# Kernel tuning notes

Hardware: AMD Instinct MI355X
Metric: run time of the kernel (lower is better)

The kernel has to match this reference:

```python
import jax, jax.numpy as jnp
import numpy as np

B, S, D, NH = 2, 1024, 2048, 8
QK, V, I = 1024, 2048, 8192  # qk_dim = D/2, v_dim = D, intermediate = 4D
CAP = 15.0
EPS = 1e-6


def setup_inputs() -> dict:
    key = jax.random.key(0)
    ks = jax.random.split(key, 12)
    sc = D ** -0.5
    return {
        "x": jax.random.normal(ks[0], (B, S, D), jnp.float32),
        "Wq": jax.random.normal(ks[1], (D, QK), jnp.float32) * sc,
        "Wk": jax.random.normal(ks[2], (D, QK), jnp.float32) * sc,
        "Wv": jax.random.normal(ks[3], (D, V), jnp.float32) * sc,
        "Wo": jax.random.normal(ks[4], (D, V), jnp.float32) * sc,
        "Wi": jax.random.normal(ks[5], (D, NH), jnp.float32) * sc,
        "bi": -10.0 * jnp.ones((NH,), jnp.float32),   # xLSTM input-gate bias init
        "Wf": jax.random.normal(ks[6], (D, NH), jnp.float32) * sc,
        "bf": jnp.linspace(3.0, 6.0, NH, dtype=jnp.float32),  # forget-gate bias init
        "mh_norm_w": jnp.ones((V,), jnp.float32),
        "Wout": jax.random.normal(ks[7], (V, D), jnp.float32) * (V ** -0.5),
        "rms1_w": jnp.ones((D,), jnp.float32),
        "Wgate": jax.random.normal(ks[8], (D, I), jnp.float32) * sc,
        "Wup": jax.random.normal(ks[9], (D, I), jnp.float32) * sc,
        "Wdown": jax.random.normal(ks[10], (I, D), jnp.float32) * (I ** -0.5),
        "rms2_w": jnp.ones((D,), jnp.float32),
    }


def soft_cap(x, cap=CAP):
    return cap * jnp.tanh(x / cap)


def rms_norm(x, w, eps=EPS):
    xf = x.astype(jnp.float32)
    var = jnp.mean(xf * xf, axis=-1, keepdims=True)
    return (w * (xf * jax.lax.rsqrt(var + eps))).astype(x.dtype)


def mlstm_stabilized(q, k, v, i, f):
    # q,k: [B,NH,S,DQK]; v: [B,NH,S,DV]; i,f: [B,NH,S] (soft-capped preacts)
    dqk = q.shape[-1]
    logf = jax.nn.log_sigmoid(f.astype(jnp.float32))
    lfc = jnp.cumsum(logf, axis=-1)                         # [B,NH,S]
    tri = jnp.tril(jnp.ones((S, S), bool))
    # log decay D[t,s] = sum_{j=s+1..t} log sig(f_j) + i_s  (causal)
    logD = jnp.where(tri, lfc[..., :, None] - lfc[..., None, :], -jnp.inf) + i[..., None, :]
    m = jnp.max(logD, axis=-1, keepdims=True)               # [B,NH,S,1] stabilizer
    Dm = jnp.exp(logD - m)
    scores = jnp.einsum("bhsd,bhtd->bhst", q, k) * (dqk ** -0.5) * Dm
    n = jnp.maximum(jnp.abs(scores.sum(-1, keepdims=True)), jnp.exp(-m))
    return jnp.einsum("bhst,bhtv->bhsv", scores, v) / (n + EPS)  # [B,NH,S,DV]


def xlstm_layer(x, Wq, Wk, Wv, Wo, Wi, bi, Wf, bf, mh_norm_w, Wout):
    q = (x @ Wq).reshape(B, S, NH, -1).transpose(0, 2, 1, 3)
    k = (x @ Wk).reshape(B, S, NH, -1).transpose(0, 2, 1, 3)
    v = (x @ Wv).reshape(B, S, NH, -1).transpose(0, 2, 1, 3)
    o_preact = x @ Wo                                       # [B,S,V]
    i = soft_cap(x @ Wi + bi).transpose(0, 2, 1)            # [B,NH,S]
    f = soft_cap(x @ Wf + bf).transpose(0, 2, 1)
    h = mlstm_stabilized(q, k, v, i, f)                     # [B,NH,S,DV]
    h = h.transpose(0, 2, 1, 3)                             # [B,S,NH,DV]
    # multi-head RMS norm over per-head value dim
    hf = h.astype(jnp.float32)
    var = jnp.mean(hf * hf, axis=-1, keepdims=True)
    hn = (hf * jax.lax.rsqrt(var + EPS)).reshape(B, S, V) * mh_norm_w
    h_out = jax.nn.sigmoid(o_preact) * hn                   # output gate
    return h_out @ Wout


def reference(x, Wq, Wk, Wv, Wo, Wi, bi, Wf, bf, mh_norm_w, Wout, rms1_w,
              Wgate, Wup, Wdown, rms2_w):
    residual = x
    h = xlstm_layer(x, Wq, Wk, Wv, Wo, Wi, bi, Wf, bf, mh_norm_w, Wout)
    h = residual + rms_norm(h, rms1_w)
    mlp = (jax.nn.silu(h @ Wgate) * (h @ Wup)) @ Wdown
    return h + rms_norm(mlp, rms2_w)
```

## Files before the change

### kernel.cpp

```cpp
#include <hip/hip_runtime.h>
#include <hip/hip_bf16.h>

#define TOKENS 2048
#define DMODEL 2048
#define SEQ    1024
#define QKVO   6144

typedef __attribute__((ext_vector_type(8))) short bf16x8;
typedef __attribute__((ext_vector_type(4))) short bf16x4;
typedef __attribute__((ext_vector_type(4))) float f32x4;
typedef __attribute__((ext_vector_type(8))) unsigned short u16x8;
typedef __attribute__((ext_vector_type(4))) unsigned short u16x4;

__device__ __forceinline__ float sigmoidf_(float x) { return 1.f / (1.f + expf(-x)); }
__device__ __forceinline__ float softcapf_(float x) { return 15.f * tanhf(x * (1.f / 15.f)); }
__device__ __forceinline__ float logsigf_(float x) {
  return (x >= 0.f) ? -log1pf(expf(-x)) : (x - log1pf(expf(x)));
}
__device__ __forceinline__ unsigned short f2bf(float f) {
  unsigned u = __builtin_bit_cast(unsigned, f);
  u += 0x7FFFu + ((u >> 16) & 1u);
  return (unsigned short)(u >> 16);
}
__device__ __forceinline__ float bf2f(unsigned short b) {
  unsigned u = ((unsigned)b) << 16;
  return __builtin_bit_cast(float, u);
}

typedef __attribute__((address_space(3))) void lds_void;
typedef const __attribute__((address_space(1))) void gmem_void;
__device__ __forceinline__ void gload16(const void* g, void* l) {
  __builtin_amdgcn_global_load_lds((gmem_void*)g, (lds_void*)l, 16, 0, 0);
}
__device__ __forceinline__ unsigned lds_off(const void* p) {
  return (unsigned)(size_t)(__attribute__((address_space(3))) const void*)p;
}

#if defined(__has_builtin)
#if __has_builtin(__builtin_amdgcn_mfma_f32_16x16x16bf16_1k)
#define HAVE_MFMA16 1
#endif
#endif

__device__ __forceinline__ f32x4 mfma16_bf16(bf16x4 a, bf16x4 b, f32x4 c) {
#ifdef HAVE_MFMA16
  return __builtin_amdgcn_mfma_f32_16x16x16bf16_1k(a, b, c, 0, 0, 0);
#else
  f32x4 d;
  asm volatile("v_mfma_f32_16x16x16_bf16 %0, %1, %2, %3"
               : "=v"(d) : "v"(a), "v"(b), "v"(c));
  return d;
#endif
}

__device__ __forceinline__ bf16x4 tr_read(unsigned addr) {
  bf16x4 d;
  asm volatile("ds_read_b64_tr_b16 %0, %1" : "=v"(d) : "v"(addr));
  return d;
}

__device__ __forceinline__ void remap_block(int& bm, int& bn) {
  const int nbx = gridDim.x, nby = gridDim.y;
  const int bid = blockIdx.y * nbx + blockIdx.x;
  const int q = (nbx * nby) >> 3;
  const int lid = (bid & 7) * q + (bid >> 3);
  bm = lid % nby;
  bn = lid / nby;
}

template <int EPI>
__global__ __launch_bounds__(512) void gemm256(
    const unsigned short* __restrict__ A, const unsigned short* __restrict__ BT,
    void* __restrict__ Cout, int M, int N, int K, int ldk) {
  __shared__ unsigned short lds[3][2][8192];
  const int tid = threadIdx.x;
  int bm, bn;
  remap_block(bm, bn);
  const int m0 = bm * 256, n0 = bn * 256;
  const int wid = tid >> 6, lane = tid & 63;
  const int wr = wid >> 2, wc = wid & 3;
  const int fr = lane & 15, fq = lane >> 4;
  const size_t kz = (size_t)blockIdx.z * K;

  const f32x4 zero = {0.f, 0.f, 0.f, 0.f};
  f32x4 acc[8][4];
#pragma unroll
  for (int m = 0; m < 8; ++m)
#pragma unroll
    for (int n = 0; n < 4; ++n) acc[m][n] = zero;

  const int sr = tid >> 2;
  const int sc = tid & 3;
  const int sgc = sc ^ ((sr + (sr >> 2)) & 3);
  const unsigned short* Asrc = A + kz + (size_t)(m0 + sr) * ldk + sgc * 8;
  const unsigned short* Bsrc = BT + kz + (size_t)(n0 + sr) * ldk + sgc * 8;
  const size_t hstep = (size_t)128 * ldk;
  const int ldst = sr * 32 + sc * 8;

  const int rsw = (fq ^ ((fr + (fr >> 2)) & 3)) * 8;
  const int arow0 = wr * 128 + fr;
  const int brow0 = wc * 64 + fr;

  auto stage = [&](int t) {
    const size_t ko = (size_t)t * 32;
    const int bs = t % 3;
    gload16(Asrc + ko, &lds[bs][0][ldst]);
    gload16(Asrc + ko + hstep, &lds[bs][0][4096 + ldst]);
    gload16(Bsrc + ko, &lds[bs][1][ldst]);
    gload16(Bsrc + ko + hstep, &lds[bs][1][4096 + ldst]);
  };

  const int NT = K >> 5;
  stage(0);
  stage(1);

  for (int t = 0; t < NT; ++t) {
    if (t + 1 < NT) {
      asm volatile("s_waitcnt vmcnt(4)" ::: "memory");
    } else {
      asm volatile("s_waitcnt vmcnt(0)" ::: "memory");
    }
    __builtin_amdgcn_s_barrier();
    if (t + 2 < NT) stage(t + 2);
    const int b = t % 3;
    const unsigned short* la = &lds[b][0][0];
    const unsigned short* lb = &lds[b][1][0];
    bf16x8 bfm[4], af[4];
#pragma unroll
    for (int n = 0; n < 4; ++n)
      bfm[n] = *(const bf16x8*)&lb[(brow0 + n * 16) * 32 + rsw];
#pragma unroll
    for (int m = 0; m < 4; ++m)
      af[m] = *(const bf16x8*)&la[(arow0 + m * 16) * 32 + rsw];
    __builtin_amdgcn_s_setprio(1);
#pragma unroll
    for (int m = 0; m < 4; ++m)
#pragma unroll
      for (int n = 0; n < 4; ++n)
        acc[m][n] = __builtin_amdgcn_mfma_f32_16x16x32_bf16(af[m], bfm[n],
                                                            acc[m][n], 0, 0, 0);
    __builtin_amdgcn_s_setprio(0);
#pragma unroll
    for (int m = 0; m < 4; ++m)
      af[m] = *(const bf16x8*)&la[(arow0 + 64 + m * 16) * 32 + rsw];
    __builtin_amdgcn_s_setprio(1);
#pragma unroll
    for (int m = 0; m < 4; ++m)
#pragma unroll
      for (int n = 0; n < 4; ++n)
        acc[4 + m][n] = __builtin_amdgcn_mfma_f32_16x16x32_bf16(
            af[m], bfm[n], acc[4 + m][n], 0, 0, 0);
    __builtin_amdgcn_s_setprio(0);
  }

  const int orow = m0 + wr * 128 + fq * 4;
  const int ocol = n0 + wc * 64 + fr;
#pragma unroll
  for (int m = 0; m < 8; ++m) {
#pragma unroll
    for (int n = 0; n < 4; ++n) {
      const int cc = ocol + n * 16;
#pragma unroll
      for (int j = 0; j < 4; ++j) {
        const int r = orow + m * 16 + j;
        float v = acc[m][n][j];
        if (EPI == 0) {
          ((float*)Cout + (size_t)blockIdx.z * M * N)[(size_t)r * N + cc] = v;
        } else {
          ((unsigned short*)Cout)[(size_t)r * N + cc] = f2bf(v);
        }
      }
    }
  }
}

__global__ __launch_bounds__(512) void gemm_dual(
    const unsigned short* __restrict__ A, const unsigned short* __restrict__ BT1,
    const unsigned short* __restrict__ BT2, unsigned short* __restrict__ Cout,
    int M, int N, int K) {
  __shared__ unsigned short lds[3][16384];
  const int tid = threadIdx.x;
  int bm, bn;
  remap_block(bm, bn);
  const int m0 = bm * 256, n0 = bn * 128;
  const int wid = tid >> 6, lane = tid & 63;
  const int wr = wid >> 2, wc = wid & 3;
  const int fr = lane & 15, fq = lane >> 4;

  const f32x4 zero = {0.f, 0.f, 0.f, 0.f};
  f32x4 acc1[8][2], acc2[8][2];
#pragma unroll
  for (int m = 0; m < 8; ++m)
#pragma unroll
    for (int n = 0; n < 2; ++n) { acc1[m][n] = zero; acc2[m][n] = zero; }

  const int sr = tid >> 2;
  const int sc = tid & 3;
  const int sgc = sc ^ ((sr + (sr >> 2)) & 3);
  const unsigned short* Asrc = A + (size_t)(m0 + sr) * K + sgc * 8;
  const unsigned short* B1src = BT1 + (size_t)(n0 + sr) * K + sgc * 8;
  const unsigned short* B2src = BT2 + (size_t)(n0 + sr) * K + sgc * 8;
  const size_t hstep = (size_t)128 * K;
  const int ldst = sr * 32 + sc * 8;

  const int rsw = (fq ^ ((fr + (fr >> 2)) & 3)) * 8;
  const int arow0 = wr * 128 + fr;
  const int brow0 = wc * 32 + fr;

  auto stage = [&](int t) {
    const size_t ko = (size_t)t * 32;
    const int bs = t % 3;
    gload16(Asrc + ko, &lds[bs][ldst]);
    gload16(Asrc + ko + hstep, &lds[bs][4096 + ldst]);
    gload16(B1src + ko, &lds[bs][8192 + ldst]);
    gload16(B2src + ko, &lds[bs][12288 + ldst]);
  };

  const int NT = K >> 5;
  stage(0);
  stage(1);

  for (int t = 0; t < NT; ++t) {
    if (t + 1 < NT) {
      asm volatile("s_waitcnt vmcnt(4)" ::: "memory");
    } else {
      asm volatile("s_waitcnt vmcnt(0)" ::: "memory");
    }
    __builtin_amdgcn_s_barrier();
    if (t + 2 < NT) stage(t + 2);
    const int b = t % 3;
    const unsigned short* la = &lds[b][0];
    bf16x8 b1[2], b2[2], af[4];
#pragma unroll
    for (int n = 0; n < 2; ++n) {
      b1[n] = *(const bf16x8*)&la[8192 + (brow0 + n * 16) * 32 + rsw];
      b2[n] = *(const bf16x8*)&la[12288 + (brow0 + n * 16) * 32 + rsw];
    }
#pragma unroll
    for (int m = 0; m < 4; ++m)
      af[m] = *(const bf16x8*)&la[(arow0 + m * 16) * 32 + rsw];
    __builtin_amdgcn_s_setprio(1);
#pragma unroll
    for (int m = 0; m < 4; ++m)
#pragma unroll
      for (int n = 0; n < 2; ++n) {
        acc1[m][n] = __builtin_amdgcn_mfma_f32_16x16x32_bf16(af[m], b1[n],
                                                             acc1[m][n], 0, 0, 0);
        acc2[m][n] = __builtin_amdgcn_mfma_f32_16x16x32_bf16(af[m], b2[n],
                                                             acc2[m][n], 0, 0, 0);
      }
    __builtin_amdgcn_s_setprio(0);
#pragma unroll
    for (int m = 0; m < 4; ++m)
      af[m] = *(const bf16x8*)&la[(arow0 + 64 + m * 16) * 32 + rsw];
    __builtin_amdgcn_s_setprio(1);
#pragma unroll
    for (int m = 0; m < 4; ++m)
#pragma unroll
      for (int n = 0; n < 2; ++n) {
        acc1[4 + m][n] = __builtin_amdgcn_mfma_f32_16x16x32_bf16(
            af[m], b1[n], acc1[4 + m][n], 0, 0, 0);
        acc2[4 + m][n] = __builtin_amdgcn_mfma_f32_16x16x32_bf16(
            af[m], b2[n], acc2[4 + m][n], 0, 0, 0);
      }
    __builtin_amdgcn_s_setprio(0);
  }

  const int orow = m0 + wr * 128 + fq * 4;
  const int ocol = n0 + wc * 32 + fr;
#pragma unroll
  for (int m = 0; m < 8; ++m) {
#pragma unroll
    for (int n = 0; n < 2; ++n) {
      const int cc = ocol + n * 16;
#pragma unroll
      for (int j = 0; j < 4; ++j) {
        const int r = orow + m * 16 + j;
        const float g = acc1[m][n][j];
        const float u = acc2[m][n][j];
        Cout[(size_t)r * N + cc] = f2bf(g * sigmoidf_(g) * u);
      }
    }
  }
}

template <int EPI>
__global__ __launch_bounds__(256) void gemm_bf16(
    const unsigned short* __restrict__ A, const unsigned short* __restrict__ BT,
    void* __restrict__ Cout, int M, int N, int K) {
  __shared__ unsigned short As[2][128 * 32];
  __shared__ unsigned short Bs[2][128 * 32];
  const int tid = threadIdx.x;
  int bm, bn;
  remap_block(bm, bn);
  const int m0 = bm * 128;
  const int n0 = bn * 128;
  const int wid = tid >> 6;
  const int lane = tid & 63;
  const int wr = wid >> 1, wc = wid & 1;
  const int fr = lane & 15, fq = lane >> 4;

  const f32x4 zero = {0.f, 0.f, 0.f, 0.f};
  f32x4 acc[4][4];
#pragma unroll
  for (int m = 0; m < 4; ++m)
#pragma unroll
    for (int n = 0; n < 4; ++n) acc[m][n] = zero;

  const int srow = tid >> 2;
  const int sc = tid & 3;
  const int sgc = sc ^ ((srow + (srow >> 2)) & 3);
  const int scol = sgc * 8;
  const unsigned short* Ag0 = A + (size_t)(m0 + srow) * K + scol;
  const unsigned short* Ag1 = A + (size_t)(m0 + 64 + srow) * K + scol;
  const unsigned short* Bg0 = BT + (size_t)(n0 + srow) * K + scol;
  const unsigned short* Bg1 = BT + (size_t)(n0 + 64 + srow) * K + scol;
  const int rsw = (fq ^ ((fr + (fr >> 2)) & 3)) * 8;

  gload16(Ag0, &As[0][tid * 8]);
  gload16(Ag1, &As[0][2048 + tid * 8]);
  gload16(Bg0, &Bs[0][tid * 8]);
  gload16(Bg1, &Bs[0][2048 + tid * 8]);
  __syncthreads();

  const int nt = K >> 5;
  for (int t = 0; t < nt; ++t) {
    const int cur = t & 1;
    if (t + 1 < nt) {
      const int k0 = (t + 1) << 5;
      gload16(Ag0 + k0, &As[cur ^ 1][tid * 8]);
      gload16(Ag1 + k0, &As[cur ^ 1][2048 + tid * 8]);
      gload16(Bg0 + k0, &Bs[cur ^ 1][tid * 8]);
      gload16(Bg1 + k0, &Bs[cur ^ 1][2048 + tid * 8]);
    }
    bf16x8 af[4], bfm[4];
#pragma unroll
    for (int m = 0; m < 4; ++m)
      af[m] = *(const bf16x8*)&As[cur][(wr * 64 + m * 16 + fr) * 32 + rsw];
#pragma unroll
    for (int n = 0; n < 4; ++n)
      bfm[n] = *(const bf16x8*)&Bs[cur][(wc * 64 + n * 16 + fr) * 32 + rsw];
    __builtin_amdgcn_s_setprio(1);
#pragma unroll
    for (int m = 0; m < 4; ++m)
#pragma unroll
      for (int n = 0; n < 4; ++n)
        acc[m][n] = __builtin_amdgcn_mfma_f32_16x16x32_bf16(af[m], bfm[n],
                                                            acc[m][n], 0, 0, 0);
    __builtin_amdgcn_s_setprio(0);
    __syncthreads();
  }

  const int orow = m0 + wr * 64 + fq * 4;
  const int ocol = n0 + wc * 64 + fr;
#pragma unroll
  for (int m = 0; m < 4; ++m) {
#pragma unroll
    for (int n = 0; n < 4; ++n) {
      const int cc = ocol + n * 16;
#pragma unroll
      for (int j = 0; j < 4; ++j) {
        const int r = orow + m * 16 + j;
        float v = acc[m][n][j];
        if (EPI == 0) ((float*)Cout)[(size_t)r * N + cc] = v;
        else ((unsigned short*)Cout)[(size_t)r * N + cc] = f2bf(v);
      }
    }
  }
}

__global__ __launch_bounds__(256) void castT_kernel(
    const float* __restrict__ W, unsigned short* __restrict__ WT, int K, int N) {
  __shared__ float tile[128][65];
  const int n0 = blockIdx.x * 64, k0 = blockIdx.y * 128;
  const int rr = threadIdx.x >> 4;
  const int c4 = (threadIdx.x & 15) * 4;
#pragma unroll
  for (int p = 0; p < 8; ++p) {
    const int r = p * 16 + rr;
    float4 v = *(const float4*)&W[(size_t)(k0 + r) * N + n0 + c4];
    tile[r][c4 + 0] = v.x; tile[r][c4 + 1] = v.y;
    tile[r][c4 + 2] = v.z; tile[r][c4 + 3] = v.w;
  }
  __syncthreads();
  const int kc = (threadIdx.x & 15) * 8;
#pragma unroll
  for (int p = 0; p < 4; ++p) {
    const int n = p * 16 + rr;
    u16x8 o;
#pragma unroll
    for (int j = 0; j < 8; ++j) o[j] = f2bf(tile[kc + j][n]);
    *(u16x8*)&WT[(size_t)(n0 + n) * K + k0 + kc] = o;
  }
}

__global__ __launch_bounds__(256) void gatesT_kernel(
    const float* __restrict__ Wi, const float* __restrict__ Wf,
    float* __restrict__ WT) {
  const int idx = blockIdx.x * 256 + threadIdx.x;
  const int row = idx >> 11;
  const int d = idx & 2047;
  const float* W = (row < 8) ? Wi : Wf;
  WT[idx] = W[d * 8 + (row & 7)];
}

__global__ __launch_bounds__(256) void gates_kernel(
    const float* __restrict__ x, const float* __restrict__ WT,
    const float* __restrict__ bi, const float* __restrict__ bf,
    float* __restrict__ icap, float* __restrict__ fls,
    unsigned short* __restrict__ xb) {
  const int t = blockIdx.x;
  const int tid = threadIdx.x;
  __shared__ float xs[2048];
  *(float4*)&xs[tid * 4] = *(const float4*)&x[(size_t)t * 2048 + tid * 4];
  *(float4*)&xs[1024 + tid * 4] =
      *(const float4*)&x[(size_t)t * 2048 + 1024 + tid * 4];
  __syncthreads();
  {
    u16x8 o;
#pragma unroll
    for (int j = 0; j < 8; ++j) o[j] = f2bf(xs[tid * 8 + j]);
    *(u16x8*)&xb[(size_t)t * 2048 + tid * 8] = o;
  }
  const int wave = tid >> 6, lane = tid & 63;
  const int b = t >> 10, s = t & 1023;
  for (int gg = wave; gg < 16; gg += 4) {
    const int head = gg & 7;
    const int isF = gg >> 3;
    const float* Wrow = WT + (size_t)gg * 2048;
    float acc = 0.f;
#pragma unroll
    for (int it = 0; it < 8; ++it) {
      const float4 w4 = *(const float4*)&Wrow[it * 256 + lane * 4];
      const float4 x4 = *(const float4*)&xs[it * 256 + lane * 4];
      acc = fmaf(x4.x, w4.x, acc);
      acc = fmaf(x4.y, w4.y, acc);
      acc = fmaf(x4.z, w4.z, acc);
      acc = fmaf(x4.w, w4.w, acc);
    }
#pragma unroll
    for (int m = 32; m > 0; m >>= 1) acc += __shfl_down(acc, m, 64);
    if (lane == 0) {
      const size_t o = (size_t)(b * 8 + head) * 1024 + s;
      if (isF) fls[o] = logsigf_(softcapf_(acc + bf[head]));
      else icap[o] = softcapf_(acc + bi[head]);
    }
  }
}

__global__ __launch_bounds__(1024) void scan_kernel(
    const float* __restrict__ icap, const float* __restrict__ fls,
    float* __restrict__ lfc, float* __restrict__ garr, float* __restrict__ mx) {
  const int bh = blockIdx.x;
  const int tid = threadIdx.x;
  __shared__ float sm[1024];
  sm[tid] = fls[(size_t)bh * 1024 + tid];
  __syncthreads();
  for (int off = 1; off < 1024; off <<= 1) {
    float v = sm[tid];
    if (tid >= off) v += sm[tid - off];
    __syncthreads();
    sm[tid] = v;
    __syncthreads();
  }
  const float l = sm[tid];
  lfc[(size_t)bh * 1024 + tid] = l;
  const float g = icap[(size_t)bh * 1024 + tid] - l;
  garr[(size_t)bh * 1024 + tid] = g;
  __syncthreads();
  sm[tid] = g;
  __syncthreads();
  for (int off = 1; off < 1024; off <<= 1) {
    float v = sm[tid];
    if (tid >= off) v = fmaxf(v, sm[tid - off]);
    __syncthreads();
    sm[tid] = v;
    __syncthreads();
  }
  mx[(size_t)bh * 1024 + tid] = sm[tid];
}

__global__ __launch_bounds__(256) void mlstm_mfma_kernel(
    const unsigned short* __restrict__ qkvob,
    const float* __restrict__ garr, const float* __restrict__ lfc,
    const float* __restrict__ mx, const float* __restrict__ mhw,
    unsigned short* __restrict__ houtb) {
  __shared__ unsigned short k_lds[32 * 128];
  __shared__ unsigned short v_lds[32 * 256];
  const int tid = threadIdx.x;
  const int lane = tid & 63;
  const int w = tid >> 6;
  const int bh = blockIdx.y;
  const int b = bh >> 3, hh = bh & 7;
  const int tb = blockIdx.x;
  const int fr = lane & 15, fq = lane >> 4;
  const int tw = tb * 64 + w * 16 + fr;
  const size_t tokT = (size_t)(b * SEQ + tw);
  const float scale = 0.08838834764831845f;

  bf16x8 qf[4];
#pragma unroll
  for (int kd = 0; kd < 4; ++kd)
    qf[kd] = *(const bf16x8*)&qkvob[tokT * QKVO + hh * 128 + kd * 32 + fq * 8];

  const float Mt = mx[(size_t)bh * SEQ + tw];
  const float mt = lfc[(size_t)bh * SEQ + tw] + Mt;

  f32x4 acc[16];
  const f32x4 zero = {0.f, 0.f, 0.f, 0.f};
#pragma unroll
  for (int D = 0; D < 16; ++D) acc[D] = zero;
  float asum = 0.f;

  const unsigned vbase = lds_off(v_lds);
  const int nsb = tb * 2 + 2;

  for (int sb = 0; sb < nsb; ++sb) {
    const int s0 = sb * 32;
    if (sb) __syncthreads();
#pragma unroll
    for (int it = 0; it < 2; ++it) {
      const int ck = it * 256 + tid;
      const int s = ck >> 4, c = ck & 15;
      const int cg = c ^ (s & 7);
      gload16(&qkvob[(size_t)(b * SEQ + s0 + s) * QKVO + 1024 + hh * 128 + cg * 8],
              &k_lds[ck * 8]);
    }
#pragma unroll
    for (int it = 0; it < 4; ++it) {
      const int cv = it * 256 + tid;
      const int W_ = cv >> 9, D = (cv >> 5) & 15, g = (cv >> 3) & 3,
                jj = (cv >> 1) & 3, c2 = cv & 1;
      const int s = W_ * 16 + g * 4 + jj;
      gload16(&qkvob[(size_t)(b * SEQ + s0 + s) * QKVO + 2048 + hh * 256 +
                     D * 16 + c2 * 8],
              &v_lds[cv * 8]);
    }
    __syncthreads();

#pragma unroll
    for (int st = 0; st < 2; ++st) {
      f32x4 cfrag = zero;
      const int srow = st * 16 + fr;
#pragma unroll
      for (int kd = 0; kd < 4; ++kd) {
        const int cc = (kd * 4 + fq) ^ (srow & 7);
        const bf16x8 kf = *(const bf16x8*)&k_lds[srow * 128 + cc * 8];
        cfrag = __builtin_amdgcn_mfma_f32_16x16x32_bf16(kf, qf[kd], cfrag, 0, 0, 0);
      }
      const int sbase = s0 + st * 16 + fq * 4;
      const float4 g4 = *(const float4*)&garr[(size_t)bh * SEQ + sbase];
      float wv[4];
      wv[0] = (sbase + 0 <= tw) ? cfrag[0] * scale * __expf(g4.x - Mt) : 0.f;
      wv[1] = (sbase + 1 <= tw) ? cfrag[1] * scale * __expf(g4.y - Mt) : 0.f;
      wv[2] = (sbase + 2 <= tw) ? cfrag[2] * scale * __expf(g4.z - Mt) : 0.f;
      wv[3] = (sbase + 3 <= tw) ? cfrag[3] * scale * __expf(g4.w - Mt) : 0.f;
      asum += wv[0] + wv[1] + wv[2] + wv[3];
      bf16x4 pf;
      pf[0] = (short)f2bf(wv[0]); pf[1] = (short)f2bf(wv[1]);
      pf[2] = (short)f2bf(wv[2]); pf[3] = (short)f2bf(wv[3]);

#pragma unroll
      for (int Dg = 0; Dg < 2; ++Dg) {
        bf16x4 vf[8];
#pragma unroll
        for (int D = 0; D < 8; ++D)
          vf[D] = tr_read(vbase + (st * 4096 + (Dg * 8 + D) * 256) * 2 + lane * 8);
        asm volatile("s_waitcnt lgkmcnt(0)" ::: "memory");
        __builtin_amdgcn_sched_barrier(0);
#pragma unroll
        for (int D = 0; D < 8; ++D)
          acc[Dg * 8 + D] = mfma16_bf16(vf[D], pf, acc[Dg * 8 + D]);
      }
    }
  }

  asum += __shfl_xor(asum, 16, 64);
  asum += __shfl_xor(asum, 32, 64);
  const float nrm = fmaxf(fabsf(asum), __expf(-mt));
  const float inv = 1.f / (nrm + 1e-6f);
  asm volatile("s_nop 7\n\ts_nop 7" ::);

  float hv[16][4];
  float ss = 0.f;
#pragma unroll
  for (int D = 0; D < 16; ++D)
#pragma unroll
    for (int j = 0; j < 4; ++j) {
      const float v = acc[D][j] * inv;
      hv[D][j] = v;
      ss += v * v;
    }
  ss += __shfl_xor(ss, 16, 64);
  ss += __shfl_xor(ss, 32, 64);
  const float rinv = rsqrtf(ss * (1.f / 256.f) + 1e-6f);
  unsigned short* hrow = &houtb[tokT * 2048 + hh * 256];
  const unsigned short* orow = &qkvob[tokT * QKVO + 4096 + hh * 256];
  const float* mrow = &mhw[hh * 256];
#pragma unroll
  for (int D = 0; D < 16; ++D) {
    const int d0 = D * 16 + fq * 4;
    const float4 m4 = *(const float4*)&mrow[d0];
    const u16x4 o4 = *(const u16x4*)&orow[d0];
    u16x4 res;
    res[0] = f2bf(hv[D][0] * rinv * m4.x * sigmoidf_(bf2f(o4[0])));
    res[1] = f2bf(hv[D][1] * rinv * m4.y * sigmoidf_(bf2f(o4[1])));
    res[2] = f2bf(hv[D][2] * rinv * m4.z * sigmoidf_(bf2f(o4[2])));
    res[3] = f2bf(hv[D][3] * rinv * m4.w * sigmoidf_(bf2f(o4[3])));
    *(u16x4*)&hrow[d0] = res;
  }
}

template <int EMIT_BF16, int NY>
__global__ __launch_bounds__(256) void addrms_kernel(
    const float* __restrict__ base_, const float* __restrict__ y0,
    const float* __restrict__ y1, const float* __restrict__ y2,
    const float* __restrict__ y3, const float* __restrict__ w,
    float* __restrict__ outp, unsigned short* __restrict__ outb) {
  const int t = blockIdx.x;
  const int tid = threadIdx.x;
  __shared__ float red[4];
  const size_t boff = (size_t)t * 2048 + tid * 8;
  float vals[8];
  *(float4*)&vals[0] = *(const float4*)&y0[boff];
  *(float4*)&vals[4] = *(const float4*)&y0[boff + 4];
  if (NY == 4) {
    float v1[8];
    *(float4*)&v1[0] = *(const float4*)&y1[boff];
    *(float4*)&v1[4] = *(const float4*)&y1[boff + 4];
#pragma unroll
    for (int j = 0; j < 8; ++j) vals[j] += v1[j];
    *(float4*)&v1[0] = *(const float4*)&y2[boff];
    *(float4*)&v1[4] = *(const float4*)&y2[boff + 4];
#pragma unroll
    for (int j = 0; j < 8; ++j) vals[j] += v1[j];
    *(float4*)&v1[0] = *(const float4*)&y3[boff];
    *(float4*)&v1[4] = *(const float4*)&y3[boff + 4];
#pragma unroll
    for (int j = 0; j < 8; ++j) vals[j] += v1[j];
  }
  float ss = 0.f;
#pragma unroll
  for (int j = 0; j < 8; ++j) ss += vals[j] * vals[j];
#pragma unroll
  for (int m = 32; m > 0; m >>= 1) ss += __shfl_xor(ss, m, 64);
  if ((tid & 63) == 0) red[tid >> 6] = ss;
  __syncthreads();
  ss = red[0] + red[1] + red[2] + red[3];
  const float rinv = rsqrtf(ss * (1.f / 2048.f) + 1e-6f);
  float bv[8];
  *(float4*)&bv[0] = *(const float4*)&base_[boff];
  *(float4*)&bv[4] = *(const float4*)&base_[boff + 4];
  float res[8];
  u16x8 rb;
#pragma unroll
  for (int j = 0; j < 8; ++j) {
    res[j] = bv[j] + vals[j] * rinv * w[tid * 8 + j];
    if (EMIT_BF16) rb[j] = f2bf(res[j]);
  }
  *(float4*)&outp[boff] = *(float4*)&res[0];
  *(float4*)&outp[boff + 4] = *(float4*)&res[4];
  if (EMIT_BF16) *(u16x8*)&outb[boff] = rb;
}

extern "C" void kernel_launch(void* const* d_in, const int* in_sizes, int n_in,
                              void* d_out, int out_size, void* d_ws,
                              size_t ws_size, hipStream_t stream) {
  const float* x = (const float*)d_in[0];
  const float* Wq = (const float*)d_in[1];
  const float* Wk = (const float*)d_in[2];
  const float* Wv = (const float*)d_in[3];
  const float* Wo = (const float*)d_in[4];
  const float* Wi = (const float*)d_in[5];
  const float* bi = (const float*)d_in[6];
  const float* Wf = (const float*)d_in[7];
  const float* bf = (const float*)d_in[8];
  const float* mhw = (const float*)d_in[9];
  const float* Wout = (const float*)d_in[10];
  const float* rms1 = (const float*)d_in[11];
  const float* Wgate = (const float*)d_in[12];
  const float* Wup = (const float*)d_in[13];
  const float* Wdown = (const float*)d_in[14];
  const float* rms2 = (const float*)d_in[15];
  float* out = (float*)d_out;
  char* base = (char*)d_ws;
  const size_t MBy = 1024 * 1024;

  unsigned short* W = (unsigned short*)(base);
  unsigned short* actb = (unsigned short*)(base + 32 * MBy);
  float* gs = (float*)(base + 48 * MBy);
  unsigned short* houtb = (unsigned short*)(base + 56 * MBy);
  float* f1 = (float*)(base + 64 * MBy);
  unsigned short* WupT = (unsigned short*)(base + 80 * MBy);
  float* mlp = (float*)(base + 80 * MBy);
  unsigned short* xb = (unsigned short*)(base + 112 * MBy);
  unsigned short* f1b = (unsigned short*)(base + 112 * MBy);
  unsigned short* qkvob = (unsigned short*)(base + 120 * MBy);
  float* attn = (float*)(base + 120 * MBy);
  float* icap = gs;
  float* fls = gs + 16384;
  float* lfc = gs + 32768;
  float* garr = gs + 49152;
  float* mxp = gs + 65536;
  float* gwT = gs + 81920;

  const dim3 blk(256);

  gatesT_kernel<<<128, blk, 0, stream>>>(Wi, Wf, gwT);
  gates_kernel<<<TOKENS, blk, 0, stream>>>(x, gwT, bi, bf, icap, fls, xb);
  scan_kernel<<<16, 1024, 0, stream>>>(icap, fls, lfc, garr, mxp);

  castT_kernel<<<dim3(16, 16), blk, 0, stream>>>(Wq, W, 2048, 1024);
  castT_kernel<<<dim3(16, 16), blk, 0, stream>>>(Wk, W + (size_t)1024 * 2048,
                                                 2048, 1024);
  castT_kernel<<<dim3(32, 16), blk, 0, stream>>>(Wv, W + (size_t)2048 * 2048,
                                                 2048, 2048);
  castT_kernel<<<dim3(32, 16), blk, 0, stream>>>(Wo, W + (size_t)4096 * 2048,
                                                 2048, 2048);
  gemm256<1><<<dim3(24, 8), dim3(512), 0, stream>>>(
      xb, W, qkvob, TOKENS, 6144, 2048, 2048);

  mlstm_mfma_kernel<<<dim3(16, 16), dim3(256), 0, stream>>>(
      qkvob, garr, lfc, mxp, mhw, houtb);

  castT_kernel<<<dim3(32, 16), blk, 0, stream>>>(Wout, W, 2048, 2048);
  gemm_bf16<0><<<dim3(16, 16), blk, 0, stream>>>(houtb, W, attn, TOKENS, 2048,
                                                 2048);

  addrms_kernel<1, 1><<<TOKENS, blk, 0, stream>>>(
      x, attn, nullptr, nullptr, nullptr, rms1, f1, f1b);

  castT_kernel<<<dim3(128, 16), blk, 0, stream>>>(Wgate, W, 2048, 8192);
  castT_kernel<<<dim3(128, 16), blk, 0, stream>>>(Wup, WupT, 2048, 8192);
  gemm_dual<<<dim3(64, 8), dim3(512), 0, stream>>>(f1b, W, WupT, actb,
                                                   TOKENS, 8192, 2048);

  castT_kernel<<<dim3(32, 64), blk, 0, stream>>>(Wdown, W, 8192, 2048);
  gemm256<0><<<dim3(8, 8, 4), dim3(512), 0, stream>>>(
      actb, W, mlp, TOKENS, 2048, 2048, 8192);

  addrms_kernel<0, 4><<<TOKENS, blk, 0, stream>>>(
      f1, mlp, mlp + 4194304, mlp + 8388608, mlp + 12582912, rms2, out,
      nullptr);
}
```

Measured before the change: 505.0 us.

## Batch weight-cast launches and split mLSTM into smaller causally-balanced blocks

Merges the four QKVO weight cast/transposes into one 3D-grid launch and the gate/up casts into another, which cuts launch overhead. The mLSTM kernel now uses 128-thread blocks covering 32 query rows each, doubling the grid to 512 blocks. Causal tile order is reversed for the second half of the batch-head rows so long and short blocks interleave across the GPU. Each block now loads whole K/V tiles with half the threads, giving more per-thread load work but better occupancy and load balance.

Result: no change. 497.1 us (-1.6%).

```diff
diff --git a/kernel.cpp b/kernel.cpp
--- a/kernel.cpp
+++ b/kernel.cpp
@@ -369,7 +369,7 @@
   }
 }
 
-__global__ __launch_bounds__(256) void castT_kernel(
+__device__ __forceinline__ void castT_body(
     const float* __restrict__ W, unsigned short* __restrict__ WT, int K, int N) {
   __shared__ float tile[128][65];
   const int n0 = blockIdx.x * 64, k0 = blockIdx.y * 128;
@@ -392,6 +392,34 @@
     for (int j = 0; j < 8; ++j) o[j] = f2bf(tile[kc + j][n]);
     *(u16x8*)&WT[(size_t)(n0 + n) * K + k0 + kc] = o;
   }
+}
+
+__global__ __launch_bounds__(256) void castT_kernel(
+    const float* __restrict__ W, unsigned short* __restrict__ WT, int K, int N) {
+  castT_body(W, WT, K, N);
+}
+
+__global__ __launch_bounds__(256) void castT4_kernel(
+    const float* __restrict__ Wq, const float* __restrict__ Wk,
+    const float* __restrict__ Wv, const float* __restrict__ Wo,
+    unsigned short* __restrict__ WT) {
+  const int z = blockIdx.z;
+  const float* src;
+  unsigned short* dst;
+  int N;
+  if (z == 0)      { src = Wq; dst = WT;                          N = 1024; }
+  else if (z == 1) { src = Wk; dst = WT + (size_t)1024 * 2048;    N = 1024; }
+  else if (z == 2) { src = Wv; dst = WT + (size_t)2048 * 2048;    N = 2048; }
+  else             { src = Wo; dst = WT + (size_t)4096 * 2048;    N = 2048; }
+  if (blockIdx.x * 64 >= N) return;
+  castT_body(src, dst, 2048, N);
+}
+
+__global__ __launch_bounds__(256) void castT2_kernel(
+    const float* __restrict__ Wgate, const float* __restrict__ Wup,
+    unsigned short* __restrict__ WT1, unsigned short* __restrict__ WT2) {
+  if (blockIdx.z == 0) castT_body(Wgate, WT1, 2048, 8192);
+  else castT_body(Wup, WT2, 2048, 8192);
 }
 
 __global__ __launch_bounds__(256) void gatesT_kernel(
@@ -480,7 +508,7 @@
   mx[(size_t)bh * 1024 + tid] = sm[tid];
 }
 
-__global__ __launch_bounds__(256) void mlstm_mfma_kernel(
+__global__ __launch_bounds__(128) void mlstm_mfma_kernel(
     const unsigned short* __restrict__ qkvob,
     const float* __restrict__ garr, const float* __restrict__ lfc,
     const float* __restrict__ mx, const float* __restrict__ mhw,
@@ -492,9 +520,9 @@
   const int w = tid >> 6;
   const int bh = blockIdx.y;
   const int b = bh >> 3, hh = bh & 7;
-  const int tb = blockIdx.x;
+  const int tb = (blockIdx.y < 8) ? blockIdx.x : (31 - blockIdx.x);
   const int fr = lane & 15, fq = lane >> 4;
-  const int tw = tb * 64 + w * 16 + fr;
+  const int tw = tb * 32 + w * 16 + fr;
   const size_t tokT = (size_t)(b * SEQ + tw);
   const float scale = 0.08838834764831845f;
 
@@ -513,22 +541,22 @@
   float asum = 0.f;
 
   const unsigned vbase = lds_off(v_lds);
-  const int nsb = tb * 2 + 2;
+  const int nsb = tb + 1;
 
   for (int sb = 0; sb < nsb; ++sb) {
     const int s0 = sb * 32;
     if (sb) __syncthreads();
 #pragma unroll
-    for (int it = 0; it < 2; ++it) {
-      const int ck = it * 256 + tid;
+    for (int it = 0; it < 4; ++it) {
+      const int ck = it * 128 + tid;
       const int s = ck >> 4, c = ck & 15;
       const int cg = c ^ (s & 7);
       gload16(&qkvob[(size_t)(b * SEQ + s0 + s) * QKVO + 1024 + hh * 128 + cg * 8],
               &k_lds[ck * 8]);
     }
 #pragma unroll
-    for (int it = 0; it < 4; ++it) {
-      const int cv = it * 256 + tid;
+    for (int it = 0; it < 8; ++it) {
+      const int cv = it * 128 + tid;
       const int W_ = cv >> 9, D = (cv >> 5) & 15, g = (cv >> 3) & 3,
                 jj = (cv >> 1) & 3, c2 = cv & 1;
       const int s = W_ * 16 + g * 4 + jj;
@@ -710,17 +738,11 @@
   gates_kernel<<<TOKENS, blk, 0, stream>>>(x, gwT, bi, bf, icap, fls, xb);
   scan_kernel<<<16, 1024, 0, stream>>>(icap, fls, lfc, garr, mxp);
 
-  castT_kernel<<<dim3(16, 16), blk, 0, stream>>>(Wq, W, 2048, 1024);
-  castT_kernel<<<dim3(16, 16), blk, 0, stream>>>(Wk, W + (size_t)1024 * 2048,
-                                                 2048, 1024);
-  castT_kernel<<<dim3(32, 16), blk, 0, stream>>>(Wv, W + (size_t)2048 * 2048,
-                                                 2048, 2048);
-  castT_kernel<<<dim3(32, 16), blk, 0, stream>>>(Wo, W + (size_t)4096 * 2048,
-                                                 2048, 2048);
+  castT4_kernel<<<dim3(32, 16, 4), blk, 0, stream>>>(Wq, Wk, Wv, Wo, W);
   gemm256<1><<<dim3(24, 8), dim3(512), 0, stream>>>(
       xb, W, qkvob, TOKENS, 6144, 2048, 2048);
 
-  mlstm_mfma_kernel<<<dim3(16, 16), dim3(256), 0, stream>>>(
+  mlstm_mfma_kernel<<<dim3(32, 16), dim3(128), 0, stream>>>(
       qkvob, garr, lfc, mxp, mhw, houtb);
 
   castT_kernel<<<dim3(32, 16), blk, 0, stream>>>(Wout, W, 2048, 2048);
@@ -730,8 +752,7 @@
   addrms_kernel<1, 1><<<TOKENS, blk, 0, stream>>>(
       x, attn, nullptr, nullptr, nullptr, rms1, f1, f1b);
 
-  castT_kernel<<<dim3(128, 16), blk, 0, stream>>>(Wgate, W, 2048, 8192);
-  castT_kernel<<<dim3(128, 16), blk, 0, stream>>>(Wup, WupT, 2048, 8192);
+  castT2_kernel<<<dim3(128, 16, 2), blk, 0, stream>>>(Wgate, Wup, W, WupT);
   gemm_dual<<<dim3(64, 8), dim3(512), 0, stream>>>(f1b, W, WupT, actb,
                                                    TOKENS, 8192, 2048);
 
```
